# Performance work log

Hardware: AMD Instinct MI355X
Metric: run time of the kernel (lower is better)

## Reference

```python
import jax, jax.numpy as jnp
import numpy as np

DIM_EMB = 1024
DIM_K = 128
DIM_V = 128
BATCH = 4
SEQ = 4096

def setup_inputs() -> dict:
    key = jax.random.key(0)
    kx, kq, kk, kv = jax.random.split(key, 4)
    x = jax.random.normal(kx, (BATCH, SEQ, DIM_EMB), dtype=jnp.float32)
    Wq = jax.random.normal(kq, (DIM_EMB, DIM_K), dtype=jnp.float32) * (1.0 / np.sqrt(DIM_EMB))
    Wk = jax.random.normal(kk, (DIM_EMB, DIM_K), dtype=jnp.float32) * (1.0 / np.sqrt(DIM_EMB))
    Wv = jax.random.normal(kv, (DIM_EMB, DIM_V), dtype=jnp.float32) * (1.0 / np.sqrt(DIM_EMB))
    return {"x": x, "Wq": Wq, "Wk": Wk, "Wv": Wv}

def reference(x, Wq, Wk, Wv):
    # x: [b, s, e]; projections (torch Linear without bias -> x @ W)
    seq_len = x.shape[1]
    q = x @ Wq  # [b, s, dk]
    k = x @ Wk  # [b, s, dk]
    v = x @ Wv  # [b, s, dv]
    # NOTE: original scales by 1/sqrt(dim_emb), not 1/sqrt(dim_k)
    scale = 1.0 / np.sqrt(x.shape[-1])
    qk = jnp.einsum('bqd,bkd->bqk', q, k) * scale  # [b, s, s]
    causal = jnp.tril(jnp.ones((seq_len, seq_len), dtype=bool))
    masked_qk = jnp.where(causal, qk, -jnp.inf)
    att = jax.nn.softmax(masked_qk, axis=-1)  # dropout p=0.0 -> identity
    return att @ v  # [b, s, dv]
```

## Files before the change

kernel.cpp:

```cpp
#include <hip/hip_runtime.h>

typedef __attribute__((ext_vector_type(8))) short s8v;
typedef __attribute__((ext_vector_type(4))) short s4v;
typedef __attribute__((ext_vector_type(4))) float f4v;

#define S_ 4096
#define E_ 1024
#define D_ 128

__device__ __forceinline__ unsigned short f2bf(float f) {
  unsigned int u = __float_as_uint(f);
  return (unsigned short)((u + 0x7FFFu + ((u >> 16) & 1u)) >> 16);
}

__device__ __forceinline__ void gload16(const void* g, void* l) {
  __builtin_amdgcn_global_load_lds(
      (const __attribute__((address_space(1))) unsigned int*)g,
      (__attribute__((address_space(3))) unsigned int*)l, 16, 0, 0);
}

__device__ __forceinline__ int slot_off(int s) { return s * (3840 - 256 * s); }

__global__ __launch_bounds__(256) void prep_kernel(
    const float* __restrict__ x, const float* __restrict__ Wq,
    const float* __restrict__ Wk, const float* __restrict__ Wv,
    unsigned short* __restrict__ Xb, unsigned short* __restrict__ Wt) {
  __shared__ unsigned short T[64][72];
  const int bid = blockIdx.x;
  if (bid < 8192) {
    const size_t i = ((size_t)bid * 256 + threadIdx.x) * 8;
    float4 a = *reinterpret_cast<const float4*>(x + i);
    float4 c = *reinterpret_cast<const float4*>(x + i + 4);
    s8v v;
    v[0] = (short)f2bf(a.x); v[1] = (short)f2bf(a.y);
    v[2] = (short)f2bf(a.z); v[3] = (short)f2bf(a.w);
    v[4] = (short)f2bf(c.x); v[5] = (short)f2bf(c.y);
    v[6] = (short)f2bf(c.z); v[7] = (short)f2bf(c.w);
    *reinterpret_cast<s8v*>(Xb + i) = v;
  } else {
    const int w = bid - 8192;
    const int p = w >> 5, bx = w & 31;
    const float* W = (p == 0) ? Wq : (p == 1) ? Wk : Wv;
    const int k0 = (bx >> 1) * 64;
    const int n0 = (bx & 1) * 64;
    const int t = threadIdx.x, rr = t >> 4, c4 = (t & 15) * 4;
#pragma unroll
    for (int i = 0; i < 4; ++i) {
      int kr = i * 16 + rr;
      float4 ww = *reinterpret_cast<const float4*>(W + (size_t)(k0 + kr) * D_ + n0 + c4);
      T[c4 + 0][kr] = f2bf(ww.x); T[c4 + 1][kr] = f2bf(ww.y);
      T[c4 + 2][kr] = f2bf(ww.z); T[c4 + 3][kr] = f2bf(ww.w);
    }
    __syncthreads();
#pragma unroll
    for (int i = 0; i < 4; ++i) {
      int n = i * 16 + rr;
      s4v v;
      v[0] = (short)T[n][c4]; v[1] = (short)T[n][c4 + 1];
      v[2] = (short)T[n][c4 + 2]; v[3] = (short)T[n][c4 + 3];
      *reinterpret_cast<s4v*>(Wt + (size_t)(p * D_ + n0 + n) * E_ + k0 + c4) = v;
    }
  }
}

__global__ __launch_bounds__(256, 3) void proj_kernel(
    const unsigned short* __restrict__ Xb, const unsigned short* __restrict__ Wt,
    unsigned short* __restrict__ Qb, unsigned short* __restrict__ Kb,
    unsigned short* __restrict__ VT) {
  __shared__ __align__(16) unsigned short As[128 * 64];
  __shared__ __align__(16) unsigned short Bs[64 * 64];
  const int bid = blockIdx.x;
  const int cls = bid & 7, j = bid >> 3;
  const int m0 = (cls * 16 + j / 6) * 128, ng = j % 6;
  const int t = threadIdx.x;
  const int wv = t >> 6, lane = t & 63, quad = lane >> 4, l16 = lane & 15;
  const int wr = wv >> 1, wc = wv & 1;

  f4v acc[4][2];
  const f4v fz = {0.f, 0.f, 0.f, 0.f};
#pragma unroll
  for (int i = 0; i < 4; ++i)
#pragma unroll
    for (int k = 0; k < 2; ++k) acc[i][k] = fz;

  const int lrow = lane >> 3;
  const int scb = ((lane & 7) ^ lrow) * 16;
  const char* aSrc = (const char*)(Xb + (size_t)(m0 + wv * 32 + lrow) * E_) + scb;
  const char* bSrc = (const char*)(Wt + (size_t)(ng * 64 + wv * 16 + lrow) * E_) + scb;
  char* aDst = (char*)As + wv * 4096;
  char* bDst = (char*)Bs + wv * 2048;

  const int xm = (l16 & 7) * 16;
  const char* Ab = (const char*)As + (wr * 64 + l16) * 128;
  const char* Bb = (const char*)Bs + (wc * 32 + l16) * 128;

  for (int kk = 0; kk < E_; kk += 64) {
#pragma unroll
    for (int i = 0; i < 4; ++i)
      gload16(aSrc + (size_t)(i * 8 * E_ + kk) * 2, aDst + i * 1024);
#pragma unroll
    for (int i = 0; i < 2; ++i)
      gload16(bSrc + (size_t)(i * 8 * E_ + kk) * 2, bDst + i * 1024);
    __syncthreads();
#pragma unroll
    for (int ks = 0; ks < 2; ++ks) {
      const int co = (ks * 64 + quad * 16) ^ xm;
      s8v af[4], bf[2];
#pragma unroll
      for (int rt = 0; rt < 4; ++rt)
        af[rt] = *reinterpret_cast<const s8v*>(Ab + rt * 2048 + co);
#pragma unroll
      for (int ct = 0; ct < 2; ++ct)
        bf[ct] = *reinterpret_cast<const s8v*>(Bb + ct * 2048 + co);
#pragma unroll
      for (int rt = 0; rt < 4; ++rt)
#pragma unroll
        for (int ct = 0; ct < 2; ++ct)
          acc[rt][ct] = __builtin_amdgcn_mfma_f32_16x16x32_bf16(
              af[rt], bf[ct], acc[rt][ct], 0, 0, 0);
    }
    __syncthreads();
  }

  const int p = ng >> 1, n0 = (ng & 1) * 64;
  if (p < 2) {
    unsigned short* dst = p ? Kb : Qb;
#pragma unroll
    for (int rt = 0; rt < 4; ++rt)
#pragma unroll
      for (int ct = 0; ct < 2; ++ct)
#pragma unroll
        for (int r = 0; r < 4; ++r)
          dst[(size_t)(m0 + wr * 64 + rt * 16 + quad * 4 + r) * D_ +
              n0 + wc * 32 + ct * 16 + l16] = f2bf(acc[rt][ct][r]);
  } else {
    const int b = m0 >> 12;
    const int s0 = (m0 & (S_ - 1)) + wr * 64;
#pragma unroll
    for (int rt = 0; rt < 4; ++rt)
#pragma unroll
      for (int ct = 0; ct < 2; ++ct) {
        s4v v;
        v[0] = (short)f2bf(acc[rt][ct][0]); v[1] = (short)f2bf(acc[rt][ct][1]);
        v[2] = (short)f2bf(acc[rt][ct][2]); v[3] = (short)f2bf(acc[rt][ct][3]);
        *reinterpret_cast<s4v*>(
            VT + ((size_t)b * D_ + n0 + wc * 32 + ct * 16 + l16) * S_ + s0 +
            rt * 16 + quad * 4) = v;
      }
  }
}

__global__ __launch_bounds__(256, 4) void flash_kernel(
    const unsigned short* __restrict__ Qb, const unsigned short* __restrict__ Kb,
    const unsigned short* __restrict__ VT, float* __restrict__ Op,
    float* __restrict__ Lp) {
  __shared__ __align__(16) unsigned short KS[64 * 128];
  __shared__ __align__(16) unsigned short VS[128 * 72];
  const int id = blockIdx.x;
  const int xcd = id & 7;
  const int b = xcd >> 1;
  const int sub = 287 - ((id >> 3) * 2 + (xcd & 1));
  int g = 0;
#pragma unroll
  for (int gg = 0; gg < 7; ++gg)
    if (sub >= 4 * (gg + 1) * (gg + 2)) g = gg + 1;
  const int off = sub - 4 * g * (g + 1);
  const int qt = 8 * g + off / (g + 1);
  const int s = off % (g + 1);
  const int q0 = qt * 64;
  const int klo = s * 512;
  const int khi = min((s + 1) * 512, (qt + 1) * 64);

  const int t = threadIdx.x;
  const int wv = t >> 6, lane = t & 63, quad = lane >> 4, l16 = lane & 15;
  const int qrow0 = q0 + wv * 16;
  const float SCL2 = 0.03125f * 1.44269504088896340736f;

  const unsigned short* Kbb = Kb + (size_t)b * S_ * D_;
  const unsigned short* Vbb = VT + (size_t)b * D_ * S_;

  s8v Qf[4];
#pragma unroll
  for (int ks = 0; ks < 4; ++ks)
    Qf[ks] = *reinterpret_cast<const s8v*>(
        Qb + ((size_t)b * S_ + qrow0 + l16) * D_ + ks * 32 + quad * 8);

  f4v O[8];
  const f4v fz = {0.f, 0.f, 0.f, 0.f};
#pragma unroll
  for (int nt = 0; nt < 8; ++nt) O[nt] = fz;
  float lt = 0.f;

  const int krow = t >> 4, kgb = t & 15;
  const int vrow = t >> 1, vgb = (t & 1) * 4;

  s8v kr[4], vr[4];
#pragma unroll
  for (int i = 0; i < 4; ++i) {
    kr[i] = *reinterpret_cast<const s8v*>(
        Kbb + (size_t)(klo + krow + 16 * i) * D_ + kgb * 8);
    vr[i] = *reinterpret_cast<const s8v*>(
        Vbb + (size_t)vrow * S_ + klo + (vgb + i) * 8);
  }

  for (int k0 = klo; k0 < khi; k0 += 64) {
    __syncthreads();
#pragma unroll
    for (int i = 0; i < 4; ++i) {
      const int r = krow + 16 * i;
      const int sig = (krow & 3) | ((((krow >> 3) + 2 * i) & 3) << 2);
      *reinterpret_cast<s8v*>(KS + r * 128 + ((kgb ^ sig) * 8)) = kr[i];
      *reinterpret_cast<s8v*>(VS + vrow * 72 + (vgb + i) * 8) = vr[i];
    }
    __syncthreads();
    if (k0 + 64 < khi) {
#pragma unroll
      for (int i = 0; i < 4; ++i) {
        kr[i] = *reinterpret_cast<const s8v*>(
            Kbb + (size_t)(k0 + 64 + krow + 16 * i) * D_ + kgb * 8);
        vr[i] = *reinterpret_cast<const s8v*>(
            Vbb + (size_t)vrow * S_ + k0 + 64 + (vgb + i) * 8);
      }
    }

    if (k0 <= qrow0 + 15) {
      f4v St[2][2];
#pragma unroll
      for (int c = 0; c < 2; ++c)
#pragma unroll
        for (int s2 = 0; s2 < 2; ++s2) St[c][s2] = fz;
      __builtin_amdgcn_s_setprio(1);
#pragma unroll
      for (int ks = 0; ks < 4; ++ks)
#pragma unroll
        for (int c = 0; c < 2; ++c)
#pragma unroll
          for (int s2 = 0; s2 < 2; ++s2) {
            const int row = c * 32 + ((l16 >> 2) << 3) + s2 * 4 + (l16 & 3);
            s8v kf = *reinterpret_cast<const s8v*>(
                KS + row * 128 + (((ks * 4 + quad) ^ l16) * 8));
            St[c][s2] = __builtin_amdgcn_mfma_f32_16x16x32_bf16(
                kf, Qf[ks], St[c][s2], 0, 0, 0);
          }
      __builtin_amdgcn_s_setprio(0);
      const bool full = (k0 + 63 <= qrow0);
      s8v pf[2];
#pragma unroll
      for (int c = 0; c < 2; ++c) {
        float ladd = 0.f;
#pragma unroll
        for (int s2 = 0; s2 < 2; ++s2)
#pragma unroll
          for (int r = 0; r < 4; ++r) {
            float e = exp2f(St[c][s2][r] * SCL2);
            if (!full) {
              int key = k0 + c * 32 + quad * 8 + s2 * 4 + r;
              if (key > qrow0 + l16) e = 0.f;
            }
            ladd += e;
            pf[c][s2 * 4 + r] = (short)f2bf(e);
          }
        lt += ladd;
      }
      __builtin_amdgcn_s_setprio(1);
#pragma unroll
      for (int c = 0; c < 2; ++c)
#pragma unroll
        for (int nt = 0; nt < 8; ++nt) {
          s8v vf = *reinterpret_cast<const s8v*>(
              VS + (nt * 16 + l16) * 72 + (c * 4 + quad) * 8);
          O[nt] = __builtin_amdgcn_mfma_f32_16x16x32_bf16(
              pf[c], vf, O[nt], 0, 0, 0);
        }
      __builtin_amdgcn_s_setprio(0);
    }
  }

  lt += __shfl_xor(lt, 16);
  lt += __shfl_xor(lt, 32);
  const int soff = slot_off(s);
#pragma unroll
  for (int nt = 0; nt < 8; ++nt)
#pragma unroll
    for (int r = 0; r < 4; ++r)
      Op[((size_t)(qrow0 + quad * 4 + r + soff) * 4 + b) * D_ + nt * 16 + l16] =
          O[nt][r];
  if (lane < 16) Lp[(size_t)(qrow0 + l16 + soff) * 4 + b] = lt;
}

__global__ __launch_bounds__(256) void norm_kernel(
    const float* __restrict__ Op, const float* __restrict__ Lp,
    float* __restrict__ out) {
  const int idx = blockIdx.x * 256 + threadIdx.x;
  const int rowg = idx >> 5, d4 = idx & 31;
  const int b = rowg >> 12, row = rowg & 4095;
  const int g = row >> 9;
  float ax = 0.f, ay = 0.f, az = 0.f, aw = 0.f, L = 0.f;
  for (int s = 0; s <= g; ++s) {
    const size_t pr = (size_t)(row + slot_off(s)) * 4 + b;
    float4 o = reinterpret_cast<const float4*>(Op + pr * D_)[d4];
    ax += o.x; ay += o.y; az += o.z; aw += o.w;
    L += Lp[pr];
  }
  float4 r;
  const float inv = 1.f / L;
  r.x = ax * inv; r.y = ay * inv; r.z = az * inv; r.w = aw * inv;
  reinterpret_cast<float4*>(out)[idx] = r;
}

extern "C" void kernel_launch(void* const* d_in, const int* in_sizes, int n_in,
                              void* d_out, int out_size, void* d_ws, size_t ws_size,
                              hipStream_t stream) {
  const float* x = (const float*)d_in[0];
  const float* Wq = (const float*)d_in[1];
  const float* Wk = (const float*)d_in[2];
  const float* Wv = (const float*)d_in[3];
  float* out = (float*)d_out;

  char* ws = (char*)d_ws;
  unsigned short* Qb = (unsigned short*)ws;
  unsigned short* Kb = (unsigned short*)(ws + (((size_t)4) << 20));
  unsigned short* VT = (unsigned short*)(ws + (((size_t)8) << 20));
  unsigned short* Wt = (unsigned short*)(ws + (((size_t)12) << 20));
  unsigned short* Xb = (unsigned short*)(ws + (((size_t)13) << 20));
  float* Op = (float*)(ws + (((size_t)13) << 20));
  float* Lp = (float*)(ws + (((size_t)50) << 20));

  prep_kernel<<<8288, 256, 0, stream>>>(x, Wq, Wk, Wv, Xb, Wt);
  proj_kernel<<<768, 256, 0, stream>>>(Xb, Wt, Qb, Kb, VT);
  flash_kernel<<<1152, 256, 0, stream>>>(Qb, Kb, VT, Op, Lp);
  norm_kernel<<<2048, 256, 0, stream>>>(Op, Lp, out);
}
```

Measured before the change: 167.8 us.

## Fuse x bf16 conversion into projection GEMM, double-buffer it, and use direct LDS loads in flash

Removes the separate pass that converted x to bf16 and wrote it to the workspace. The projection GEMM now reads fp32 x, converts it in registers with packed bf16 conversion instructions, and stores it into double-buffered LDS, with one barrier per k-step. The flash kernel loads K and V straight into swizzled LDS using global_load_lds instead of register staging, shrinks the V tile padding, raises the occupancy hint, and packs P with cvt_pk. The trade-off is that x is now read as fp32 once per column group (six times) instead of once, and the flash K/V loads are no longer prefetched across iterations.

```diff
diff --git a/kernel.cpp b/kernel.cpp
--- a/kernel.cpp
+++ b/kernel.cpp
@@ -11,6 +11,12 @@
 __device__ __forceinline__ unsigned short f2bf(float f) {
   unsigned int u = __float_as_uint(f);
   return (unsigned short)((u + 0x7FFFu + ((u >> 16) & 1u)) >> 16);
+}
+
+__device__ __forceinline__ unsigned int cvtpk(float lo, float hi) {
+  unsigned int r;
+  asm("v_cvt_pk_bf16_f32 %0, %1, %2" : "=v"(r) : "v"(lo), "v"(hi));
+  return r;
 }
 
 __device__ __forceinline__ void gload16(const void* g, void* l) {
@@ -22,53 +28,39 @@
 __device__ __forceinline__ int slot_off(int s) { return s * (3840 - 256 * s); }
 
 __global__ __launch_bounds__(256) void prep_kernel(
-    const float* __restrict__ x, const float* __restrict__ Wq,
-    const float* __restrict__ Wk, const float* __restrict__ Wv,
-    unsigned short* __restrict__ Xb, unsigned short* __restrict__ Wt) {
+    const float* __restrict__ Wq, const float* __restrict__ Wk,
+    const float* __restrict__ Wv, unsigned short* __restrict__ Wt) {
   __shared__ unsigned short T[64][72];
-  const int bid = blockIdx.x;
-  if (bid < 8192) {
-    const size_t i = ((size_t)bid * 256 + threadIdx.x) * 8;
-    float4 a = *reinterpret_cast<const float4*>(x + i);
-    float4 c = *reinterpret_cast<const float4*>(x + i + 4);
-    s8v v;
-    v[0] = (short)f2bf(a.x); v[1] = (short)f2bf(a.y);
-    v[2] = (short)f2bf(a.z); v[3] = (short)f2bf(a.w);
-    v[4] = (short)f2bf(c.x); v[5] = (short)f2bf(c.y);
-    v[6] = (short)f2bf(c.z); v[7] = (short)f2bf(c.w);
-    *reinterpret_cast<s8v*>(Xb + i) = v;
-  } else {
-    const int w = bid - 8192;
-    const int p = w >> 5, bx = w & 31;
-    const float* W = (p == 0) ? Wq : (p == 1) ? Wk : Wv;
-    const int k0 = (bx >> 1) * 64;
-    const int n0 = (bx & 1) * 64;
-    const int t = threadIdx.x, rr = t >> 4, c4 = (t & 15) * 4;
-#pragma unroll
-    for (int i = 0; i < 4; ++i) {
-      int kr = i * 16 + rr;
-      float4 ww = *reinterpret_cast<const float4*>(W + (size_t)(k0 + kr) * D_ + n0 + c4);
-      T[c4 + 0][kr] = f2bf(ww.x); T[c4 + 1][kr] = f2bf(ww.y);
-      T[c4 + 2][kr] = f2bf(ww.z); T[c4 + 3][kr] = f2bf(ww.w);
-    }
-    __syncthreads();
-#pragma unroll
-    for (int i = 0; i < 4; ++i) {
-      int n = i * 16 + rr;
-      s4v v;
-      v[0] = (short)T[n][c4]; v[1] = (short)T[n][c4 + 1];
-      v[2] = (short)T[n][c4 + 2]; v[3] = (short)T[n][c4 + 3];
-      *reinterpret_cast<s4v*>(Wt + (size_t)(p * D_ + n0 + n) * E_ + k0 + c4) = v;
-    }
+  const int w = blockIdx.x;
+  const int p = w >> 5, bx = w & 31;
+  const float* W = (p == 0) ? Wq : (p == 1) ? Wk : Wv;
+  const int k0 = (bx >> 1) * 64;
+  const int n0 = (bx & 1) * 64;
+  const int t = threadIdx.x, rr = t >> 4, c4 = (t & 15) * 4;
+#pragma unroll
+  for (int i = 0; i < 4; ++i) {
+    int kr = i * 16 + rr;
+    float4 ww = *reinterpret_cast<const float4*>(W + (size_t)(k0 + kr) * D_ + n0 + c4);
+    T[c4 + 0][kr] = f2bf(ww.x); T[c4 + 1][kr] = f2bf(ww.y);
+    T[c4 + 2][kr] = f2bf(ww.z); T[c4 + 3][kr] = f2bf(ww.w);
+  }
+  __syncthreads();
+#pragma unroll
+  for (int i = 0; i < 4; ++i) {
+    int n = i * 16 + rr;
+    s4v v;
+    v[0] = (short)T[n][c4]; v[1] = (short)T[n][c4 + 1];
+    v[2] = (short)T[n][c4 + 2]; v[3] = (short)T[n][c4 + 3];
+    *reinterpret_cast<s4v*>(Wt + (size_t)(p * D_ + n0 + n) * E_ + k0 + c4) = v;
   }
 }
 
 __global__ __launch_bounds__(256, 3) void proj_kernel(
-    const unsigned short* __restrict__ Xb, const unsigned short* __restrict__ Wt,
+    const float* __restrict__ x, const unsigned short* __restrict__ Wt,
     unsigned short* __restrict__ Qb, unsigned short* __restrict__ Kb,
     unsigned short* __restrict__ VT) {
-  __shared__ __align__(16) unsigned short As[128 * 64];
-  __shared__ __align__(16) unsigned short Bs[64 * 64];
+  __shared__ __align__(16) unsigned short As[2][128 * 64];
+  __shared__ __align__(16) unsigned short Bs[2][64 * 64];
   const int bid = blockIdx.x;
   const int cls = bid & 7, j = bid >> 3;
   const int m0 = (cls * 16 + j / 6) * 128, ng = j % 6;
@@ -83,25 +75,46 @@
 #pragma unroll
     for (int k = 0; k < 2; ++k) acc[i][k] = fz;
 
+  const int ar = t >> 1, khalf = t & 1;
+  const float* xg = x + (size_t)(m0 + ar) * E_ + khalf * 32;
+
   const int lrow = lane >> 3;
   const int scb = ((lane & 7) ^ lrow) * 16;
-  const char* aSrc = (const char*)(Xb + (size_t)(m0 + wv * 32 + lrow) * E_) + scb;
   const char* bSrc = (const char*)(Wt + (size_t)(ng * 64 + wv * 16 + lrow) * E_) + scb;
-  char* aDst = (char*)As + wv * 4096;
-  char* bDst = (char*)Bs + wv * 2048;
 
   const int xm = (l16 & 7) * 16;
-  const char* Ab = (const char*)As + (wr * 64 + l16) * 128;
-  const char* Bb = (const char*)Bs + (wc * 32 + l16) * 128;
-
-  for (int kk = 0; kk < E_; kk += 64) {
-#pragma unroll
-    for (int i = 0; i < 4; ++i)
-      gload16(aSrc + (size_t)(i * 8 * E_ + kk) * 2, aDst + i * 1024);
-#pragma unroll
-    for (int i = 0; i < 2; ++i)
-      gload16(bSrc + (size_t)(i * 8 * E_ + kk) * 2, bDst + i * 1024);
+
+  float4 xa[8];
+#pragma unroll
+  for (int m = 0; m < 8; ++m) xa[m] = *reinterpret_cast<const float4*>(xg + 4 * m);
+#pragma unroll
+  for (int i = 0; i < 2; ++i)
+    gload16(bSrc + (size_t)(i * 8 * E_) * 2, (char*)Bs[0] + wv * 2048 + i * 1024);
+
+  int buf = 0;
+  for (int kk = 0; kk < E_; kk += 64, buf ^= 1) {
+#pragma unroll
+    for (int j2 = 0; j2 < 4; ++j2) {
+      union { unsigned int u[4]; s8v v; } gv;
+      gv.u[0] = cvtpk(xa[2 * j2].x, xa[2 * j2].y);
+      gv.u[1] = cvtpk(xa[2 * j2].z, xa[2 * j2].w);
+      gv.u[2] = cvtpk(xa[2 * j2 + 1].x, xa[2 * j2 + 1].y);
+      gv.u[3] = cvtpk(xa[2 * j2 + 1].z, xa[2 * j2 + 1].w);
+      const int g = khalf * 4 + j2;
+      *reinterpret_cast<s8v*>((char*)As[buf] + ar * 128 + ((g ^ (ar & 7)) * 16)) = gv.v;
+    }
     __syncthreads();
+    if (kk + 64 < E_) {
+#pragma unroll
+      for (int m = 0; m < 8; ++m)
+        xa[m] = *reinterpret_cast<const float4*>(xg + kk + 64 + 4 * m);
+#pragma unroll
+      for (int i = 0; i < 2; ++i)
+        gload16(bSrc + (size_t)(i * 8 * E_ + kk + 64) * 2,
+                (char*)Bs[buf ^ 1] + wv * 2048 + i * 1024);
+    }
+    const char* Ab = (const char*)As[buf] + (wr * 64 + l16) * 128;
+    const char* Bb = (const char*)Bs[buf] + (wc * 32 + l16) * 128;
 #pragma unroll
     for (int ks = 0; ks < 2; ++ks) {
       const int co = (ks * 64 + quad * 16) ^ xm;
@@ -119,7 +132,6 @@
           acc[rt][ct] = __builtin_amdgcn_mfma_f32_16x16x32_bf16(
               af[rt], bf[ct], acc[rt][ct], 0, 0, 0);
     }
-    __syncthreads();
   }
 
   const int p = ng >> 1, n0 = (ng & 1) * 64;
@@ -150,12 +162,12 @@
   }
 }
 
-__global__ __launch_bounds__(256, 4) void flash_kernel(
+__global__ __launch_bounds__(256, 5) void flash_kernel(
     const unsigned short* __restrict__ Qb, const unsigned short* __restrict__ Kb,
     const unsigned short* __restrict__ VT, float* __restrict__ Op,
     float* __restrict__ Lp) {
   __shared__ __align__(16) unsigned short KS[64 * 128];
-  __shared__ __align__(16) unsigned short VS[128 * 72];
+  __shared__ __align__(16) unsigned short VS[128 * 64];
   const int id = blockIdx.x;
   const int xcd = id & 7;
   const int b = xcd >> 1;
@@ -191,37 +203,20 @@
   for (int nt = 0; nt < 8; ++nt) O[nt] = fz;
   float lt = 0.f;
 
-  const int krow = t >> 4, kgb = t & 15;
-  const int vrow = t >> 1, vgb = (t & 1) * 4;
-
-  s8v kr[4], vr[4];
-#pragma unroll
-  for (int i = 0; i < 4; ++i) {
-    kr[i] = *reinterpret_cast<const s8v*>(
-        Kbb + (size_t)(klo + krow + 16 * i) * D_ + kgb * 8);
-    vr[i] = *reinterpret_cast<const s8v*>(
-        Vbb + (size_t)vrow * S_ + klo + (vgb + i) * 8);
-  }
-
   for (int k0 = klo; k0 < khi; k0 += 64) {
     __syncthreads();
 #pragma unroll
     for (int i = 0; i < 4; ++i) {
-      const int r = krow + 16 * i;
-      const int sig = (krow & 3) | ((((krow >> 3) + 2 * i) & 3) << 2);
-      *reinterpret_cast<s8v*>(KS + r * 128 + ((kgb ^ sig) * 8)) = kr[i];
-      *reinterpret_cast<s8v*>(VS + vrow * 72 + (vgb + i) * 8) = vr[i];
+      const int ci = wv * 4 + i;
+      const int kr = ci * 4 + (lane >> 4);
+      const int sg = (kr & 3) | (((((kr >> 3) & 1) + 2 * (kr >> 4)) & 3) << 2);
+      gload16(Kbb + (size_t)(k0 + kr) * D_ + (((lane & 15) ^ sg) * 8),
+              (char*)KS + ci * 1024);
+      const int dv = ci * 8 + (lane >> 3);
+      gload16(Vbb + (size_t)dv * S_ + k0 + (((lane & 7) ^ (dv & 7)) * 8),
+              (char*)VS + ci * 1024);
     }
     __syncthreads();
-    if (k0 + 64 < khi) {
-#pragma unroll
-      for (int i = 0; i < 4; ++i) {
-        kr[i] = *reinterpret_cast<const s8v*>(
-            Kbb + (size_t)(k0 + 64 + krow + 16 * i) * D_ + kgb * 8);
-        vr[i] = *reinterpret_cast<const s8v*>(
-            Vbb + (size_t)vrow * S_ + k0 + 64 + (vgb + i) * 8);
-      }
-    }
 
     if (k0 <= qrow0 + 15) {
       f4v St[2][2];
@@ -247,20 +242,25 @@
       s8v pf[2];
 #pragma unroll
       for (int c = 0; c < 2; ++c) {
+        float e[8];
         float ladd = 0.f;
 #pragma unroll
         for (int s2 = 0; s2 < 2; ++s2)
 #pragma unroll
           for (int r = 0; r < 4; ++r) {
-            float e = exp2f(St[c][s2][r] * SCL2);
+            float ev = exp2f(St[c][s2][r] * SCL2);
             if (!full) {
               int key = k0 + c * 32 + quad * 8 + s2 * 4 + r;
-              if (key > qrow0 + l16) e = 0.f;
+              if (key > qrow0 + l16) ev = 0.f;
             }
-            ladd += e;
-            pf[c][s2 * 4 + r] = (short)f2bf(e);
+            e[s2 * 4 + r] = ev;
+            ladd += ev;
           }
         lt += ladd;
+        union { unsigned int u[4]; s8v v; } P;
+        P.u[0] = cvtpk(e[0], e[1]); P.u[1] = cvtpk(e[2], e[3]);
+        P.u[2] = cvtpk(e[4], e[5]); P.u[3] = cvtpk(e[6], e[7]);
+        pf[c] = P.v;
       }
       __builtin_amdgcn_s_setprio(1);
 #pragma unroll
@@ -268,7 +268,8 @@
 #pragma unroll
         for (int nt = 0; nt < 8; ++nt) {
           s8v vf = *reinterpret_cast<const s8v*>(
-              VS + (nt * 16 + l16) * 72 + (c * 4 + quad) * 8);
+              (const char*)VS + (nt * 16 + l16) * 128 +
+              (((c * 4 + quad) ^ (l16 & 7)) * 16));
           O[nt] = __builtin_amdgcn_mfma_f32_16x16x32_bf16(
               pf[c], vf, O[nt], 0, 0, 0);
         }
@@ -322,12 +323,11 @@
   unsigned short* Kb = (unsigned short*)(ws + (((size_t)4) << 20));
   unsigned short* VT = (unsigned short*)(ws + (((size_t)8) << 20));
   unsigned short* Wt = (unsigned short*)(ws + (((size_t)12) << 20));
-  unsigned short* Xb = (unsigned short*)(ws + (((size_t)13) << 20));
   float* Op = (float*)(ws + (((size_t)13) << 20));
   float* Lp = (float*)(ws + (((size_t)50) << 20));
 
-  prep_kernel<<<8288, 256, 0, stream>>>(x, Wq, Wk, Wv, Xb, Wt);
-  proj_kernel<<<768, 256, 0, stream>>>(Xb, Wt, Qb, Kb, VT);
+  prep_kernel<<<96, 256, 0, stream>>>(Wq, Wk, Wv, Wt);
+  proj_kernel<<<768, 256, 0, stream>>>(x, Wt, Qb, Kb, VT);
   flash_kernel<<<1152, 256, 0, stream>>>(Qb, Kb, VT, Op, Lp);
   norm_kernel<<<2048, 256, 0, stream>>>(Op, Lp, out);
 }
```

Result: slower. 204.5 us (+21.9%).
